# Optimization experiments

Hardware: AMD Instinct MI355X
Metric: run time of the kernel (lower is better)

The kernel has to match this reference:

```python
import jax, jax.numpy as jnp
import numpy as np

B, N, C, D = 2, 6, 64, 40
FH, FW = 12, 33
IMG_H, IMG_W = 384, 1056
NX, NY, NZ = 100, 100, 4
LOWER = np.array([-50.0, -50.0, -10.0], np.float32)   # xbound[0], ybound[0], zbound[0]
DXV = np.array([1.0, 1.0, 5.0], np.float32)           # voxel sizes


def _conv(x, w, pad):
    return jax.lax.conv_general_dilated(x, w, (1, 1), [(pad, pad), (pad, pad)],
                                        dimension_numbers=('NCHW', 'OIHW', 'NCHW'))


def _bn(x, s, b):
    return x * s[None, :, None, None] + b[None, :, None, None]


def _se(x, w1, b1, w2, b2):
    m = x.mean((2, 3))                                   # global avg pool -> (B, C)
    g = jax.nn.sigmoid(jax.nn.silu(m @ w1.T + b1) @ w2.T + b2)
    return x * g[:, :, None, None]


def _frustum():
    ds = jnp.arange(4.0, 44.0, 1.0)                      # (D,) depth bins
    xs = jnp.linspace(0.0, IMG_W - 1.0, FW)
    ys = jnp.linspace(0.0, IMG_H - 1.0, FH)
    f = jnp.stack(jnp.broadcast_arrays(xs[None, None, :], ys[None, :, None], ds[:, None, None]), -1)
    return f.reshape(-1, 3)                              # (D*FH*FW, 3) in (x_px, y_px, depth)


def reference(feats, rots, trans, intrinsics, nw1, bn1s, bn1b, se1w1, se1b1, se1w2, se1b2,
              nw2, bn2s, bn2b, dhw, dhb, chw, chb, bcw1, bcs1, bcb1, bcsw1, bcsb1, bcsw2,
              bcsb2, bcw2, bcs2, bcb2, dw1, ds1, db1, dw2, db2):
    BN = B * N
    # ---- CamEncoderV2 neck + heads (backbone 1280ch@1/32 features given directly) ----
    x = jax.nn.silu(_bn(_conv(feats, nw1, 0), bn1s, bn1b))
    x = _se(x, se1w1, se1b1, se1w2, se1b2)
    x = jax.nn.silu(_bn(_conv(x, nw2, 1), bn2s, bn2b))
    depth = jax.nn.softmax(_conv(x, dhw, 0) + dhb[None, :, None, None], axis=1)  # (BN, D, FH, FW)
    ctx = _conv(x, chw, 0) + chb[None, :, None, None]                            # (BN, C, FH, FW)
    # ---- geometry: pixel frustum -> ego-frame points ----
    rots_f = rots.reshape(BN, 3, 3)
    trans_f = trans.reshape(BN, 3)
    K = intrinsics.reshape(BN, 3, 3)
    pts = _frustum()                                     # (P0, 3), P0 = D*FH*FW
    d = pts[:, 2]
    fx, fy = K[:, 0, 0][:, None], K[:, 1, 1][:, None]
    cx, cy = K[:, 0, 2][:, None], K[:, 1, 2][:, None]
    cam = jnp.stack([(pts[None, :, 0] - cx) * d[None, :] / fx,
                     (pts[None, :, 1] - cy) * d[None, :] / fy,
                     jnp.broadcast_to(d[None, :], (BN, d.shape[0]))], -1)        # (BN, P0, 3)
    geom = jnp.einsum('bij,bpj->bpi', rots_f, cam) + trans_f[:, None, :]
    geom = geom.reshape(B, -1, 3)                        # (B, N*P0, 3)
    # ---- lift: outer product context x depth ----
    ff = (ctx[:, None, :, :, :] * depth[:, :, None, :, :])                       # (BN, D, C, FH, FW)
    ff = ff.transpose(0, 1, 3, 4, 2).reshape(B, -1, C)                           # (B, N*P0, C)
    # ---- splat: voxel pooling (scatter-add into BEV grid) ----
    idx = jnp.floor((geom - jnp.asarray(LOWER)) / jnp.asarray(DXV)).astype(jnp.int32)
    valid = jnp.all((idx >= 0) & (idx < jnp.array([NX, NY, NZ])), axis=-1)
    sid = idx[..., 2] * (NX * NY) + idx[..., 0] * NY + idx[..., 1]
    sid = jnp.where(valid, sid, 0)
    ffm = ff * valid[..., None]
    pooled = jax.vmap(lambda f, i: jax.ops.segment_sum(f, i, num_segments=NZ * NX * NY))(ffm, sid)
    bev = pooled.reshape(B, NZ, NX, NY, C).transpose(0, 1, 4, 2, 3).reshape(B, NZ * C, NX, NY)
    # ---- BEVCompressorV2 (residual conv-SE-conv) ----
    h = jax.nn.relu(_bn(_conv(bev, bcw1, 1), bcs1, bcb1))
    h = _se(h, bcsw1, bcsb1, bcsw2, bcsb2)
    h = jax.nn.relu(_bn(_conv(h, bcw2, 1), bcs2, bcb2))
    bev = bev + h
    # ---- decoder ----
    h = jax.nn.relu(_bn(_conv(bev, dw1, 1), ds1, db1))
    out = _conv(h, dw2, 0) + db2[None, :, None, None]    # (B, nz*num_classes, NX, NY)
    return out.reshape(B, 4, NZ, NX, NY)


def setup_inputs():
    f32 = jnp.float32
    ks = jax.random.split(jax.random.key(0), 16)
    feats = jax.random.normal(ks[0], (B * N, 1280, FH, FW), f32) * 0.5
    # cam->ego: z_cam -> x_ego, -x_cam -> y_ego, -y_cam -> z_ego, plus per-camera yaw
    Rbase = np.array([[0., 0., 1.], [-1., 0., 0.], [0., -1., 0.]], np.float32)
    yaw = np.deg2rad(np.arange(N) * 60.0).astype(np.float32)
    c, s = np.cos(yaw), np.sin(yaw)
    Rz = np.zeros((N, 3, 3), np.float32)
    Rz[:, 0, 0] = c; Rz[:, 0, 1] = -s; Rz[:, 1, 0] = s; Rz[:, 1, 1] = c; Rz[:, 2, 2] = 1.0
    rots = jnp.asarray(np.broadcast_to(np.einsum('nij,jk->nik', Rz, Rbase), (B, N, 3, 3)).copy())
    trans = jax.random.normal(ks[1], (B, N, 3), f32) * 1.0
    K = np.array([[800., 0., 528.], [0., 800., 192.], [0., 0., 1.]], np.float32)
    intrinsics = jnp.asarray(np.broadcast_to(K, (B, N, 3, 3)).copy())

    def w(k, shape, fan_in):
        return jax.random.normal(k, shape, f32) * np.float32(np.sqrt(2.0 / fan_in))

    kk = jax.random.split(ks[2], 16)
    return dict(
        feats=feats, rots=rots, trans=trans, intrinsics=intrinsics,
        nw1=w(kk[0], (256, 1280, 1, 1), 1280), bn1s=jnp.ones(256, f32), bn1b=jnp.zeros(256, f32),
        se1w1=w(kk[1], (32, 256), 256), se1b1=jnp.zeros(32, f32),
        se1w2=w(kk[2], (256, 32), 32), se1b2=jnp.zeros(256, f32),
        nw2=w(kk[3], (256, 256, 3, 3), 2304), bn2s=jnp.ones(256, f32), bn2b=jnp.zeros(256, f32),
        dhw=w(kk[4], (40, 256, 1, 1), 256), dhb=jnp.zeros(40, f32),
        chw=w(kk[5], (64, 256, 1, 1), 256), chb=jnp.zeros(64, f32),
        bcw1=w(kk[6], (256, 256, 3, 3), 2304), bcs1=jnp.ones(256, f32), bcb1=jnp.zeros(256, f32),
        bcsw1=w(kk[7], (16, 256), 256), bcsb1=jnp.zeros(16, f32),
        bcsw2=w(kk[8], (256, 16), 16), bcsb2=jnp.zeros(256, f32),
        bcw2=w(kk[9], (256, 256, 3, 3), 2304), bcs2=jnp.ones(256, f32), bcb2=jnp.zeros(256, f32),
        dw1=w(kk[10], (128, 256, 3, 3), 2304), ds1=jnp.ones(128, f32), db1=jnp.zeros(128, f32),
        dw2=w(kk[11], (16, 128, 1, 1), 128), db2=jnp.zeros(16, f32),
    )
```

## Files before the change

### kernel.cpp

```cpp
#include <hip/hip_runtime.h>
#include <hip/hip_bf16.h>
#include <cmath>


typedef __attribute__((ext_vector_type(8))) short short8;
typedef __attribute__((ext_vector_type(4))) float floatx4;
typedef __hip_bfloat16 hb;

__device__ __forceinline__ float sigf(float x){ return 1.0f/(1.0f+expf(-x)); }
__device__ __forceinline__ float siluf(float x){ return x*sigf(x); }
__device__ __forceinline__ void split2(float v, hb* h, hb* l){
  hb hv = __float2bfloat16(v);
  *h = hv; *l = __float2bfloat16(v - __bfloat162float(hv));
}

__global__ __launch_bounds__(256) void k_trans_featsP(
    const float* __restrict__ feats, hb* __restrict__ Fph, hb* __restrict__ Fpl)
{
  __shared__ float tile[64][65];
  int n = blockIdx.z;
  int p0 = blockIdx.x*64;
  int c0 = blockIdx.y*64;
  int tid = threadIdx.x;
  int tr = tid >> 6;
  int tc = tid & 63;
  #pragma unroll
  for (int it=0; it<16; ++it){
    int ci = c0 + it*4 + tr;
    int p = p0 + tc;
    float v = 0.f;
    if (p < 396) v = feats[((size_t)n*1280 + ci)*396 + p];
    tile[it*4+tr][tc] = v;
  }
  __syncthreads();
  #pragma unroll
  for (int iter=0; iter<2; ++iter){
    int idx = iter*256 + tid;
    int oc = idx >> 6;
    int pl = idx & 63;
    int p = p0 + pl;
    if (p < 396){
      int P = n*396 + p;
      int T = P >> 4, mm = P & 15;
      int kb = (c0 >> 5) + (oc >> 2);
      int q = oc & 3;
      int lane = q*16 + mm;
      size_t o = (((size_t)T*40 + kb)*64 + lane)*8;
      #pragma unroll
      for (int j=0; j<8; ++j){
        hb hv, lv; split2(tile[oc*8+j][pl], &hv, &lv);
        Fph[o+j] = hv; Fpl[o+j] = lv;
      }
    }
  }
}

__global__ __launch_bounds__(256) void k_wpackE(
    const float* __restrict__ nw1, const float* __restrict__ nw2,
    hb* __restrict__ Wc1h, hb* __restrict__ Wc1l,
    hb* __restrict__ Wc2h, hb* __restrict__ Wc2l)
{
  int i = blockIdx.x*256 + threadIdx.x;
  if (i < 327680){
    int j = i & 7;
    int lane = (i>>3) & 63;
    int t2 = i >> 9;
    int nb = t2 & 15;
    int kb = t2 >> 4;
    int ci = kb*32 + (lane>>4)*8 + j;
    int co = nb*16 + (lane&15);
    hb hv, lv; split2(nw1[(size_t)co*1280 + ci], &hv, &lv);
    Wc1h[i] = hv; Wc1l[i] = lv;
  } else {
    int i2 = i - 327680;
    if (i2 >= 589824) return;
    int j = i2 & 7;
    int t1 = i2 >> 3;
    int lane = t1 & 63;
    int t2 = t1 >> 6;
    int nb = t2 % 16;
    int t3 = t2 / 16;
    int tap = t3 % 9;
    int kb = t3 / 9;
    int ci = kb*32 + (lane>>4)*8 + j;
    int co = nb*16 + (lane&15);
    hb hv, lv; split2(nw2[(size_t)co*2304 + ci*9 + tap], &hv, &lv);
    Wc2h[i2] = hv; Wc2l[i2] = lv;
  }
}

__global__ __launch_bounds__(256) void k_wpackT3(
    const float* __restrict__ bcw1, const float* __restrict__ bcw2,
    const float* __restrict__ dw1,
    hb* __restrict__ W1h, hb* __restrict__ W1l,
    hb* __restrict__ W2h, hb* __restrict__ W2l,
    hb* __restrict__ W3h, hb* __restrict__ W3l)
{
  int gi = blockIdx.x*256 + threadIdx.x;
  const float* W; hb* Wh; hb* Wl; int NB; int i;
  if (gi < 589824){ W = bcw1; Wh = W1h; Wl = W1l; NB = 16; i = gi; }
  else if (gi < 1179648){ W = bcw2; Wh = W2h; Wl = W2l; NB = 16; i = gi - 589824; }
  else if (gi < 1474560){ W = dw1; Wh = W3h; Wl = W3l; NB = 8; i = gi - 1179648; }
  else return;
  int j = i & 7;
  int t1 = i >> 3;
  int lane = t1 & 63;
  int t2 = t1 >> 6;
  int nb = t2 % NB;
  int t3 = t2 / NB;
  int tap = t3 % 9;
  int kb = t3 / 9;
  int ci = kb*32 + (lane>>4)*8 + j;
  int co = nb*16 + (lane&15);
  hb hv, lv; split2(W[(size_t)co*2304 + ci*9 + tap], &hv, &lv);
  Wh[i] = hv; Wl[i] = lv;
}

__global__ __launch_bounds__(256) void k_wpackH(
    const float* __restrict__ dhw, const float* __restrict__ chw,
    hb* __restrict__ Wph, hb* __restrict__ Wpl)
{
  int i = blockIdx.x*256 + threadIdx.x;
  if (i >= 8*7*512) return;
  int j = i & 7;
  int t1 = i >> 3;
  int lane = t1 & 63;
  int t2 = t1 >> 6;
  int nb = t2 % 7;
  int kb = t2 / 7;
  int ci = kb*32 + (lane>>4)*8 + j;
  int co = nb*16 + (lane&15);
  float w = 0.f;
  if (co < 40) w = dhw[(size_t)co*256 + ci];
  else if (co < 104) w = chw[(size_t)(co-40)*256 + ci];
  hb hv, lv; split2(w, &hv, &lv);
  Wph[i] = hv; Wpl[i] = lv;
}

__global__ __launch_bounds__(256) void k_mfma_gemm1(
    const hb* __restrict__ Fph, const hb* __restrict__ Fpl,
    const hb* __restrict__ Wph, const hb* __restrict__ Wpl,
    const float* __restrict__ bns, const float* __restrict__ bnb,
    float* __restrict__ out)
{
  __shared__ short8 lbh[256], lbl[256];
  int tid = threadIdx.x;
  int wv = tid >> 6, lane = tid & 63;
  int cog = blockIdx.y;
  int Pbase = blockIdx.x*128 + wv*32;
  int q = lane >> 4;
  int T0 = blockIdx.x*8 + wv*2; if (T0 > 296) T0 = 296;
  int T1 = T0 + 1;              if (T1 > 296) T1 = 296;
  size_t a0 = (size_t)T0*2560 + lane;
  size_t a1 = (size_t)T1*2560 + lane;
  const short8* gAh = (const short8*)(const void*)Fph;
  const short8* gAl = (const short8*)(const void*)Fpl;
  const short8* gWh = (const short8*)(const void*)Wph;
  const short8* gWl = (const short8*)(const void*)Wpl;
  size_t sb = (size_t)(cog*4 + wv)*64 + lane;
  floatx4 acc[2][4];
  #pragma unroll
  for (int i=0;i<2;++i)
    #pragma unroll
    for (int j=0;j<4;++j) acc[i][j] = (floatx4)(0.f);
  short8 ph = gWh[sb], pw = gWl[sb];
  short8 cah0 = gAh[a0], cal0 = gAl[a0], cah1 = gAh[a1], cal1 = gAl[a1];
  for (int kb=0; kb<40; ++kb){
    __syncthreads();
    lbh[tid] = ph; lbl[tid] = pw;
    int nx = (kb+1 < 40) ? kb+1 : 39;
    ph = gWh[(size_t)nx*1024 + sb]; pw = gWl[(size_t)nx*1024 + sb];
    __syncthreads();
    short8 nah0 = gAh[a0 + (size_t)nx*64];
    short8 nal0 = gAl[a0 + (size_t)nx*64];
    short8 nah1 = gAh[a1 + (size_t)nx*64];
    short8 nal1 = gAl[a1 + (size_t)nx*64];
    #pragma unroll
    for (int nb=0; nb<4; ++nb){
      short8 bh = lbh[nb*64 + lane];
      short8 bl = lbl[nb*64 + lane];
      acc[0][nb] = __builtin_amdgcn_mfma_f32_16x16x32_bf16(cah0, bh, acc[0][nb], 0,0,0);
      acc[0][nb] = __builtin_amdgcn_mfma_f32_16x16x32_bf16(cah0, bl, acc[0][nb], 0,0,0);
      acc[0][nb] = __builtin_amdgcn_mfma_f32_16x16x32_bf16(cal0, bh, acc[0][nb], 0,0,0);
      acc[1][nb] = __builtin_amdgcn_mfma_f32_16x16x32_bf16(cah1, bh, acc[1][nb], 0,0,0);
      acc[1][nb] = __builtin_amdgcn_mfma_f32_16x16x32_bf16(cah1, bl, acc[1][nb], 0,0,0);
      acc[1][nb] = __builtin_amdgcn_mfma_f32_16x16x32_bf16(cal1, bh, acc[1][nb], 0,0,0);
    }
    cah0 = nah0; cal0 = nal0; cah1 = nah1; cal1 = nal1;
  }
  int n16 = lane & 15;
  #pragma unroll
  for (int mg=0; mg<2; ++mg){
    #pragma unroll
    for (int nb=0; nb<4; ++nb){
      int co = cog*64 + nb*16 + n16;
      float s = bns[co], bv = bnb[co];
      #pragma unroll
      for (int r=0; r<4; ++r){
        int P = Pbase + mg*16 + q*4 + r;
        if (P < 4752) out[(size_t)P*256 + co] = siluf(acc[mg][nb][r]*s + bv);
      }
    }
  }
}

__global__ __launch_bounds__(256) void k_meanse(
    const float* __restrict__ x1, const float* __restrict__ w1, const float* __restrict__ b1,
    const float* __restrict__ w2, const float* __restrict__ b2, float* __restrict__ g)
{
  __shared__ float m[256];
  __shared__ float h[32];
  int n = blockIdx.x; int t = threadIdx.x;
  float s = 0.f;
  for (int p=0; p<396; ++p) s += x1[((size_t)n*396+p)*256 + t];
  m[t] = s*(1.f/396.f);
  __syncthreads();
  if (t < 32){
    float s2 = b1[t];
    for (int c=0; c<256; ++c) s2 += m[c]*w1[t*256+c];
    h[t] = siluf(s2);
  }
  __syncthreads();
  float s3 = b2[t];
  for (int j=0; j<32; ++j) s3 += h[j]*w2[t*32+j];
  g[n*256+t] = sigf(s3);
}

__global__ __launch_bounds__(256) void k_se_fc(
    const float* __restrict__ mean, const float* __restrict__ w1, const float* __restrict__ b1,
    const float* __restrict__ w2, const float* __restrict__ b2, float* __restrict__ g, int H)
{
  __shared__ float m[256];
  __shared__ float h[32];
  int n = blockIdx.x; int t = threadIdx.x;
  m[t] = mean[n*256 + t];
  __syncthreads();
  if (t < H){
    float s = b1[t];
    for (int c=0; c<256; ++c) s += m[c]*w1[t*256+c];
    h[t] = siluf(s);
  }
  __syncthreads();
  float s = b2[t];
  for (int j=0; j<H; ++j) s += h[j]*w2[t*H+j];
  g[n*256+t] = sigf(s);
}

__global__ __launch_bounds__(256) void k_topad(
    const float* __restrict__ x1, const float* __restrict__ g,
    hb* __restrict__ Xh, hb* __restrict__ Xl)
{
  int y = blockIdx.x;
  int n = blockIdx.y;
  int c = threadIdx.x;
  float gc = g[n*256+c];
  for (int xx=0; xx<35; ++xx){
    float v = 0.f;
    if (y>=1 && y<=12 && xx>=1 && xx<=33)
      v = x1[((size_t)n*396 + (y-1)*33 + (xx-1))*256 + c]*gc;
    hb hv, lv; split2(v, &hv, &lv);
    size_t o = (((size_t)n*14+y)*35+xx)*256 + c;
    Xh[o] = hv; Xl[o] = lv;
  }
}

__global__ __launch_bounds__(256) void k_conv3_img(
    const hb* __restrict__ Xh, const hb* __restrict__ Xl,
    const hb* __restrict__ Wph, const hb* __restrict__ Wpl,
    const float* __restrict__ bns, const float* __restrict__ bnb,
    hb* __restrict__ outh, hb* __restrict__ outl)
{
  __shared__ __align__(16) short sAh[10*18*44];
  __shared__ __align__(16) short sAl[10*18*44];
  __shared__ short8 lbh[2][256], lbl[2][256];
  int tid = threadIdx.x;
  int wv = tid >> 6, lane = tid & 63;
  int xg = blockIdx.x;
  int n = blockIdx.y >> 1, yg = blockIdx.y & 1;
  int cog = blockIdx.z;
  int x0 = xg*16;
  int y0 = yg*8 + wv;
  int m = lane & 15, q = lane >> 4;
  floatx4 acc[2][4];
  #pragma unroll
  for (int i=0;i<2;++i)
    #pragma unroll
    for (int j=0;j<4;++j) acc[i][j] = (floatx4)(0.f);

  const short8* gAh = (const short8*)(const void*)Xh;
  const short8* gAl = (const short8*)(const void*)Xl;
  const short8* gWh = (const short8*)(const void*)Wph;
  const short8* gWl = (const short8*)(const void*)Wpl;
  const size_t sb = (size_t)(cog*4 + wv)*64 + lane;
  const size_t nbase = (size_t)n*14*35*32;

  short8 ph = gWh[sb], pl = gWl[sb];
  int cur = 0;

  for (int kb=0; kb<8; ++kb){
    #pragma unroll 3
    for (int tap=0; tap<9; ++tap){
      int idx2 = kb*9 + tap;
      if (tap == 0){
        __syncthreads();
        for (int i = tid; i < 720; i += 256){
          int rc = i >> 2, part = i & 3;
          int r = rc / 18, c2 = rc % 18;
          int yr = yg*8 + r; if (yr > 13) yr = 13;
          int xc = x0 + c2;  if (xc > 34) xc = 34;
          size_t so = nbase + (size_t)(yr*35 + xc)*32 + kb*4 + part;
          short8 vh = gAh[so], vl = gAl[so];
          int dst = (r*18 + c2)*44 + part*8;
          *(short8*)(sAh + dst) = vh;
          *(short8*)(sAl + dst) = vl;
        }
      }
      lbh[cur][tid] = ph; lbl[cur][tid] = pl;
      int nx = (idx2+1 < 72) ? idx2+1 : 71;
      ph = gWh[(size_t)nx*1024 + sb];
      pl = gWl[(size_t)nx*1024 + sb];
      __syncthreads();
      int dy = (tap*11) >> 5;
      int dx = tap - dy*3;
      int cc = dx + m;
      int a0 = ((wv + dy)*18 + cc)*44 + q*8;
      int a1 = ((wv + 4 + dy)*18 + cc)*44 + q*8;
      short8 cah0 = *(const short8*)(sAh + a0);
      short8 cal0 = *(const short8*)(sAl + a0);
      short8 cah1 = *(const short8*)(sAh + a1);
      short8 cal1 = *(const short8*)(sAl + a1);
      #pragma unroll
      for (int nb=0; nb<4; ++nb){
        short8 bh = lbh[cur][nb*64 + lane];
        short8 bl = lbl[cur][nb*64 + lane];
        acc[0][nb] = __builtin_amdgcn_mfma_f32_16x16x32_bf16(cah0, bh, acc[0][nb], 0,0,0);
        acc[0][nb] = __builtin_amdgcn_mfma_f32_16x16x32_bf16(cah0, bl, acc[0][nb], 0,0,0);
        acc[0][nb] = __builtin_amdgcn_mfma_f32_16x16x32_bf16(cal0, bh, acc[0][nb], 0,0,0);
        acc[1][nb] = __builtin_amdgcn_mfma_f32_16x16x32_bf16(cah1, bh, acc[1][nb], 0,0,0);
        acc[1][nb] = __builtin_amdgcn_mfma_f32_16x16x32_bf16(cah1, bl, acc[1][nb], 0,0,0);
        acc[1][nb] = __builtin_amdgcn_mfma_f32_16x16x32_bf16(cal1, bh, acc[1][nb], 0,0,0);
      }
      cur ^= 1;
    }
  }

  int n16 = lane & 15;
  #pragma unroll
  for (int mg=0; mg<2; ++mg){
    int oy = y0 + mg*4;
    if (oy < 12){
      #pragma unroll
      for (int r=0; r<4; ++r){
        int ox = x0 + q*4 + r;
        if (ox < 33){
          int P = n*396 + oy*33 + ox;
          #pragma unroll
          for (int nb=0; nb<4; ++nb){
            int co = cog*64 + nb*16 + n16;
            float v = siluf(acc[mg][nb][r]*bns[co] + bnb[co]);
            hb hv, lv; split2(v, &hv, &lv);
            outh[(size_t)P*256 + co] = hv;
            outl[(size_t)P*256 + co] = lv;
          }
        }
      }
    }
  }
}

__global__ __launch_bounds__(256) void k_headsM(
    const hb* __restrict__ x2h, const hb* __restrict__ x2l,
    const hb* __restrict__ Whh, const hb* __restrict__ Whl,
    const float* __restrict__ dhb, const float* __restrict__ chb,
    float* __restrict__ dep, float* __restrict__ ctx2)
{
  __shared__ short8 lbh[256], lbl[256];
  int tid = threadIdx.x;
  int wv = tid >> 6, lane = tid & 63;
  int cog = blockIdx.y;
  int nb0 = cog*4;
  int nbN = cog ? 3 : 4;
  int Pbase = blockIdx.x*128 + wv*32;
  int m = lane & 15, q = lane >> 4;
  int P0 = Pbase + m;      if (P0 > 4751) P0 = 4751;
  int P1 = Pbase + 16 + m; if (P1 > 4751) P1 = 4751;
  size_t rA0 = (size_t)P0*32 + q;
  size_t rA1 = (size_t)P1*32 + q;
  const short8* gAh = (const short8*)(const void*)x2h;
  const short8* gAl = (const short8*)(const void*)x2l;
  const short8* gWh = (const short8*)(const void*)Whh;
  const short8* gWl = (const short8*)(const void*)Whl;
  floatx4 acc[2][4];
  #pragma unroll
  for (int i=0;i<2;++i)
    #pragma unroll
    for (int j=0;j<4;++j) acc[i][j] = (floatx4)(0.f);
  for (int kb=0; kb<8; ++kb){
    __syncthreads();
    for (int i=tid; i<nbN*64; i+=256){
      lbh[i] = gWh[(size_t)(kb*7 + nb0)*64 + i];
      lbl[i] = gWl[(size_t)(kb*7 + nb0)*64 + i];
    }
    __syncthreads();
    short8 ah0 = gAh[rA0 + kb*4], al0 = gAl[rA0 + kb*4];
    short8 ah1 = gAh[rA1 + kb*4], al1 = gAl[rA1 + kb*4];
    for (int nb=0; nb<nbN; ++nb){
      short8 bh = lbh[nb*64 + lane];
      short8 bl = lbl[nb*64 + lane];
      acc[0][nb] = __builtin_amdgcn_mfma_f32_16x16x32_bf16(ah0, bh, acc[0][nb], 0,0,0);
      acc[0][nb] = __builtin_amdgcn_mfma_f32_16x16x32_bf16(ah0, bl, acc[0][nb], 0,0,0);
      acc[0][nb] = __builtin_amdgcn_mfma_f32_16x16x32_bf16(al0, bh, acc[0][nb], 0,0,0);
      acc[1][nb] = __builtin_amdgcn_mfma_f32_16x16x32_bf16(ah1, bh, acc[1][nb], 0,0,0);
      acc[1][nb] = __builtin_amdgcn_mfma_f32_16x16x32_bf16(ah1, bl, acc[1][nb], 0,0,0);
      acc[1][nb] = __builtin_amdgcn_mfma_f32_16x16x32_bf16(al1, bh, acc[1][nb], 0,0,0);
    }
  }
  int n16 = lane & 15;
  #pragma unroll
  for (int mg=0; mg<2; ++mg){
    #pragma unroll
    for (int r=0; r<4; ++r){
      int P = Pbase + mg*16 + q*4 + r;
      if (P < 4752){
        int nn = P/396, pim = P%396;
        for (int nb=0; nb<nbN; ++nb){
          int co = cog*64 + nb*16 + n16;
          float v = acc[mg][nb][r];
          if (co < 40)
            dep[((size_t)nn*40 + co)*396 + pim] = v + dhb[co];
          else if (co < 104)
            ctx2[((size_t)nn*396 + pim)*64 + (co-40)] = v + chb[co-40];
        }
      }
    }
  }
}

__global__ __launch_bounds__(256) void k_softmax40(float* __restrict__ dep)
{
  int i = blockIdx.x*256 + threadIdx.x;
  if (i >= 12*396) return;
  int n = i/396, p = i%396;
  float* base = dep + (size_t)n*40*396 + p;
  float mx = -1e30f;
  for (int d=0; d<40; ++d) mx = fmaxf(mx, base[(size_t)d*396]);
  float s = 0.f;
  for (int d=0; d<40; ++d){ float e = expf(base[(size_t)d*396]-mx); base[(size_t)d*396]=e; s+=e; }
  float inv = 1.f/s;
  for (int d=0; d<40; ++d) base[(size_t)d*396] *= inv;
}

__global__ __launch_bounds__(256) void k_geom(
    const float* __restrict__ rots, const float* __restrict__ trans,
    const float* __restrict__ intr, int* __restrict__ vox, int* __restrict__ cnt)
{
  int pt = blockIdx.x*256 + threadIdx.x;
  if (pt >= 190080) return;
  int b = pt/95040; int r = pt%95040;
  int n = r/15840;  int r2 = r%15840;
  int d = r2/396;   int pim = r2%396;
  int y = pim/33, x = pim%33;
  int bn = b*6+n;
  const float* R = rots + (size_t)bn*9;
  const float* T = trans + (size_t)bn*3;
  const float* K = intr + (size_t)bn*9;
  float fx=K[0], cx=K[2], fy=K[4], cy=K[5];
  float xs = (float)x * 32.96875f;
  float ys = (float)((double)y * (383.0/11.0));
  float dv = 4.0f + (float)d;
  float camx = (xs-cx)*dv/fx;
  float camy = (ys-cy)*dv/fy;
  float gx = R[0]*camx + R[1]*camy + R[2]*dv + T[0];
  float gy = R[3]*camx + R[4]*camy + R[5]*dv + T[1];
  float gz = R[6]*camx + R[7]*camy + R[8]*dv + T[2];
  int ix = (int)floorf(gx + 50.f);
  int iy = (int)floorf(gy + 50.f);
  int iz = (int)floorf((gz + 10.f)/5.f);
  bool valid = (ix>=0 && ix<100 && iy>=0 && iy<100 && iz>=0 && iz<4);
  int sid = iz*10000 + ix*100 + iy;
  vox[pt] = valid ? sid : -1;
  if (valid) atomicAdd(&cnt[b*40000 + sid], 1);
}

__global__ __launch_bounds__(256) void k_scan1(
    const int* __restrict__ cnt, int* __restrict__ off, int* __restrict__ bsum)
{
  __shared__ int s[256];
  int t = threadIdx.x;
  int i = blockIdx.x*256 + t;
  int v = (i < 80000) ? cnt[i] : 0;
  s[t] = v; __syncthreads();
  for (int o=1;o<256;o<<=1){
    int x = (t>=o) ? s[t-o] : 0;
    __syncthreads();
    s[t] += x;
    __syncthreads();
  }
  if (i < 80000) off[i] = s[t] - v;
  if (t == 255) bsum[blockIdx.x] = s[255];
}

__global__ void k_scan2(int* __restrict__ bsum, int nblk)
{
  int lane = threadIdx.x & 63;
  int run = 0;
  for (int base=0; base<nblk; base+=64){
    int i = base + lane;
    int v = (i < nblk) ? bsum[i] : 0;
    int s = v;
    #pragma unroll
    for (int o=1;o<64;o<<=1){
      int t = __shfl_up(s, o);
      if (lane >= o) s += t;
    }
    int total = __shfl(s, 63);
    if (i < nblk) bsum[i] = run + s - v;
    run += total;
  }
}

__global__ __launch_bounds__(256) void k_scan3(
    int* __restrict__ off, const int* __restrict__ bsum, int* __restrict__ cur)
{
  int i = blockIdx.x*256 + threadIdx.x;
  if (i >= 80000) return;
  int o = off[i] + bsum[i>>8];
  off[i] = o;
  cur[i] = o;
}

__global__ __launch_bounds__(256) void k_fill(
    const int* __restrict__ vox, int* __restrict__ cur, int* __restrict__ list)
{
  int pt = blockIdx.x*256 + threadIdx.x;
  if (pt >= 190080) return;
  int s = vox[pt];
  if (s < 0) return;
  int b = pt/95040;
  int slot = atomicAdd(&cur[b*40000 + s], 1);
  list[slot] = pt;
}

__global__ __launch_bounds__(256) void k_zero_ring(hb* __restrict__ Ah, hb* __restrict__ Al)
{
  int i = blockIdx.x*256 + threadIdx.x;
  if (i >= 2*404*256) return;
  int c = i & 255;
  int t = i >> 8;
  int b = t / 404;
  int ridx = t % 404;
  int py, px;
  if (ridx < 102){ py = 0; px = ridx; }
  else if (ridx < 204){ py = 101; px = ridx-102; }
  else if (ridx < 304){ py = ridx-204+1; px = 0; }
  else { py = ridx-304+1; px = 101; }
  size_t o = (((size_t)b*102 + py)*102 + px)*256 + c;
  hb z = __float2bfloat16(0.f);
  Ah[o] = z; Al[o] = z;
}

__global__ __launch_bounds__(256) void k_gather(
    const int* __restrict__ off, const int* __restrict__ cnt, const int* __restrict__ list,
    const float* __restrict__ ctx2, const float* __restrict__ dep, float* __restrict__ bev,
    hb* __restrict__ Ah, hb* __restrict__ Al)
{
  int tid = threadIdx.x;
  int bv = blockIdx.x*4 + (tid>>6);
  int c = tid & 63;
  int b = bv/40000, sid = bv%40000;
  int st = off[bv], nn = cnt[bv];
  float s = 0.f;
  for (int k=0;k<nn;++k){
    int pt = list[st+k];
    int r = pt%95040;
    int bn = b*6 + r/15840;
    int r2 = r%15840;
    int dd = r2/396, pim = r2%396;
    s += ctx2[((size_t)bn*396+pim)*64 + c] * dep[((size_t)bn*40+dd)*396 + pim];
  }
  int iz = sid/10000, rem = sid%10000;
  bev[(size_t)b*2560000 + (size_t)iz*640000 + (size_t)c*10000 + rem] = s;
  int ix = rem/100, iy = rem%100;
  size_t oh = (((size_t)b*102 + (ix+1))*102 + (iy+1))*256 + iz*64 + c;
  hb hv, lv; split2(s, &hv, &lv);
  Ah[oh] = hv; Al[oh] = lv;
}

__global__ __launch_bounds__(256) void k_tohwc2(
    const float* __restrict__ in, hb* __restrict__ Ah, hb* __restrict__ Al,
    const float* __restrict__ g)
{
  __shared__ float tile[32*105];
  int py = blockIdx.x;
  int b  = blockIdx.y;
  int cg = blockIdx.z;
  int tid = threadIdx.x;
  bool inner = (py >= 1 && py <= 100);
  if (inner){
    if (tid < 64){ int cil = tid & 31; int col = (tid>>5) ? 101 : 0; tile[cil*105 + col] = 0.f; }
    for (int i = tid; i < 3200; i += 256){
      int cil = i / 100, x = i % 100;
      int ci = cg*32 + cil;
      tile[cil*105 + (x+1)] = in[(((size_t)b*256 + ci)*100 + (py-1))*100 + x];
    }
  }
  __syncthreads();
  for (int i = tid; i < 32*102; i += 256){
    int px = i >> 5, cil = i & 31;
    int ci = cg*32 + cil;
    float v = 0.f;
    if (inner){
      v = tile[cil*105 + px];
      if (g) v *= g[b*256 + ci];
    }
    hb hv, lv; split2(v, &hv, &lv);
    size_t o = (((size_t)b*102 + py)*102 + px)*256 + ci;
    Ah[o] = hv; Al[o] = lv;
  }
}

__global__ __launch_bounds__(256) void k_rowmean(
    const float* __restrict__ in, float* __restrict__ out, int rowlen, float inv)
{
  __shared__ float ws[4];
  int row = blockIdx.x; int t = threadIdx.x;
  const float* p = in + (size_t)row*rowlen;
  float s = 0.f;
  for (int i=t; i<rowlen; i+=256) s += p[i];
  #pragma unroll
  for (int off=32; off; off>>=1) s += __shfl_down(s, off);
  if ((t&63)==0) ws[t>>6] = s;
  __syncthreads();
  if (t==0) out[row] = (ws[0]+ws[1]+ws[2]+ws[3]) * inv;
}

__global__ __launch_bounds__(256) void k_conv3_bevm(
    const hb* __restrict__ Ah, const hb* __restrict__ Al,
    const hb* __restrict__ Wph, const hb* __restrict__ Wpl,
    const float* __restrict__ bns, const float* __restrict__ bnb,
    const float* __restrict__ res, float* __restrict__ out, int Cout, int NBG)
{
  __shared__ __align__(16) short sAh[10*18*44];
  __shared__ __align__(16) short sAl[10*18*44];
  const int NB = Cout >> 4;
  int tid = threadIdx.x;
  int wv = tid >> 6, lane = tid & 63;
  int wc = wv & 1;
  int wy = wv >> 1;
  int L = blockIdx.x;
  int spatial = L / (NBG*2);
  int rem = L % (NBG*2);
  int cog = rem % NBG;
  int bb  = rem / NBG;
  int xg = spatial % 7, yg = spatial / 7;
  int x0 = xg*16;
  int m = lane & 15, q = lane >> 4;
  int nb0 = cog*4 + wc*2;
  floatx4 acc[4][2];
  #pragma unroll
  for (int r=0;r<4;++r)
    #pragma unroll
    for (int u=0;u<2;++u) acc[r][u] = (floatx4)(0.f);

  const short8* gAh = (const short8*)(const void*)Ah;
  const short8* gAl = (const short8*)(const void*)Al;
  const short8* gWh = (const short8*)(const void*)Wph;
  const short8* gWl = (const short8*)(const void*)Wpl;
  const size_t nbstride = (size_t)NB*64;

  short8 pbh[2], pbl[2];
  #pragma unroll
  for (int u=0;u<2;++u){
    pbh[u] = gWh[(size_t)(nb0+u)*64 + lane];
    pbl[u] = gWl[(size_t)(nb0+u)*64 + lane];
  }

  for (int kb=0; kb<8; ++kb){
    __syncthreads();
    for (int i = tid; i < 720; i += 256){
      int rc = i >> 2, part = i & 3;
      int r = rc / 18, c = rc % 18;
      int yr = yg*8 + r; if (yr > 101) yr = 101;
      int xc = x0 + c;   if (xc > 101) xc = 101;
      size_t so = ((size_t)((bb*102 + yr)*102 + xc))*32 + kb*4 + part;
      short8 vh = gAh[so], vl = gAl[so];
      int dst = (r*18 + c)*44 + part*8;
      *(short8*)(sAh + dst) = vh;
      *(short8*)(sAl + dst) = vl;
    }
    __syncthreads();
    #pragma unroll 3
    for (int tap=0; tap<9; ++tap){
      int idx2 = kb*9 + tap;
      short8 cbh0 = pbh[0], cbh1 = pbh[1];
      short8 cbl0 = pbl[0], cbl1 = pbl[1];
      int nx = (idx2+1 < 72) ? idx2+1 : 71;
      #pragma unroll
      for (int u=0;u<2;++u){
        pbh[u] = gWh[(size_t)nx*nbstride + (size_t)(nb0+u)*64 + lane];
        pbl[u] = gWl[(size_t)nx*nbstride + (size_t)(nb0+u)*64 + lane];
      }
      int dy = (tap*11) >> 5;
      int dx = tap - dy*3;
      int cc = dx + m;
      #pragma unroll
      for (int r=0; r<4; ++r){
        int a0 = ((wy*4 + r + dy)*18 + cc)*44 + q*8;
        short8 cah = *(const short8*)(sAh + a0);
        short8 cal = *(const short8*)(sAl + a0);
        acc[r][0] = __builtin_amdgcn_mfma_f32_16x16x32_bf16(cah, cbh0, acc[r][0], 0,0,0);
        acc[r][0] = __builtin_amdgcn_mfma_f32_16x16x32_bf16(cah, cbl0, acc[r][0], 0,0,0);
        acc[r][0] = __builtin_amdgcn_mfma_f32_16x16x32_bf16(cal, cbh0, acc[r][0], 0,0,0);
        acc[r][1] = __builtin_amdgcn_mfma_f32_16x16x32_bf16(cah, cbh1, acc[r][1], 0,0,0);
        acc[r][1] = __builtin_amdgcn_mfma_f32_16x16x32_bf16(cah, cbl1, acc[r][1], 0,0,0);
        acc[r][1] = __builtin_amdgcn_mfma_f32_16x16x32_bf16(cal, cbh1, acc[r][1], 0,0,0);
      }
    }
  }

  int n = lane & 15;
  int xq = x0 + q*4;
  #pragma unroll
  for (int r=0; r<4; ++r){
    int yo = yg*8 + wy*4 + r;
    if (yo < 100 && xq < 100){
      #pragma unroll
      for (int u=0; u<2; ++u){
        int co = (nb0+u)*16 + n;
        float s = bns[co], bv = bnb[co];
        floatx4 a = acc[r][u];
        float4 v;
        v.x = fmaxf(a[0]*s+bv, 0.f);
        v.y = fmaxf(a[1]*s+bv, 0.f);
        v.z = fmaxf(a[2]*s+bv, 0.f);
        v.w = fmaxf(a[3]*s+bv, 0.f);
        size_t o = ((size_t)(bb*Cout+co)*100 + yo)*100 + xq;
        if (res){
          float4 rv = *(const float4*)(res + o);
          v.x += rv.x; v.y += rv.y; v.z += rv.z; v.w += rv.w;
        }
        *(float4*)(out + o) = v;
      }
    }
  }
}

__global__ __launch_bounds__(256) void k_final2(
    const float* __restrict__ h, const float* __restrict__ W, const float* __restrict__ bias,
    float* __restrict__ out)
{
  __shared__ float wsl[2048];
  __shared__ float bs[16];
  int tid = threadIdx.x;
  int b = blockIdx.y;
  for (int i=tid; i<2048; i+=256) wsl[i] = W[i];
  if (tid < 16) bs[tid] = bias[tid];
  __syncthreads();
  int pix = blockIdx.x*256 + tid;
  if (pix >= 10000) return;
  float acc[16];
  #pragma unroll
  for (int oc=0; oc<16; ++oc) acc[oc] = bs[oc];
  const float* hb_ = h + (size_t)b*128*10000 + pix;
  for (int ci=0; ci<128; ++ci){
    float hv = hb_[(size_t)ci*10000];
    #pragma unroll
    for (int oc=0; oc<16; ++oc) acc[oc] += hv * wsl[oc*128 + ci];
  }
  #pragma unroll
  for (int oc=0; oc<16; ++oc)
    out[((size_t)(b*16+oc))*10000 + pix] = acc[oc];
}

extern "C" void kernel_launch(void* const* d_in, const int* in_sizes, int n_in,
                              void* d_out, int out_size, void* d_ws, size_t ws_size,
                              hipStream_t stream)
{
  (void)in_sizes; (void)n_in; (void)out_size; (void)ws_size;
  const float* feats = (const float*)d_in[0];
  const float* rots  = (const float*)d_in[1];
  const float* trans = (const float*)d_in[2];
  const float* intr  = (const float*)d_in[3];
  const float* nw1   = (const float*)d_in[4];
  const float* bn1s  = (const float*)d_in[5];
  const float* bn1b  = (const float*)d_in[6];
  const float* se1w1 = (const float*)d_in[7];
  const float* se1b1 = (const float*)d_in[8];
  const float* se1w2 = (const float*)d_in[9];
  const float* se1b2 = (const float*)d_in[10];
  const float* nw2   = (const float*)d_in[11];
  const float* bn2s  = (const float*)d_in[12];
  const float* bn2b  = (const float*)d_in[13];
  const float* dhw   = (const float*)d_in[14];
  const float* dhb   = (const float*)d_in[15];
  const float* chw   = (const float*)d_in[16];
  const float* chb   = (const float*)d_in[17];
  const float* bcw1  = (const float*)d_in[18];
  const float* bcs1  = (const float*)d_in[19];
  const float* bcb1  = (const float*)d_in[20];
  const float* bcsw1 = (const float*)d_in[21];
  const float* bcsb1 = (const float*)d_in[22];
  const float* bcsw2 = (const float*)d_in[23];
  const float* bcsb2 = (const float*)d_in[24];
  const float* bcw2  = (const float*)d_in[25];
  const float* bcs2  = (const float*)d_in[26];
  const float* bcb2  = (const float*)d_in[27];
  const float* dw1   = (const float*)d_in[28];
  const float* ds1   = (const float*)d_in[29];
  const float* db1   = (const float*)d_in[30];
  const float* dw2   = (const float*)d_in[31];
  const float* db2   = (const float*)d_in[32];
  float* out = (float*)d_out;

  float* ws = (float*)d_ws;
  float* bev   = ws;
  float* h1    = ws + 5120000;
  hb*    Ah    = (hb*)(ws + 10240000);
  hb*    Al    = (hb*)(ws + 12903424);
  float* x2    = ws + 15566848;
  float* S5    = ws + 16783360;
  float* dep   = ws + 17373184;
  float* ctx2  = ws + 17563264;
  float* mean1 = ws + 17867392;
  float* g1    = mean1 + 3072;
  float* mean2 = g1 + 3072;
  float* g2    = mean2 + 512;
  int*   vox   = (int*)(ws + 17875584);
  hb* Fph  = (hb*)bev;
  hb* Wc1h = (hb*)(bev + 3041280);
  hb* Wc1l = (hb*)(bev + 3205120);
  float* x1 = h1;
  hb* Fpl  = (hb*)(h1 + 1216512);
  hb* Xh   = (hb*)Ah;
  hb* Xl   = (hb*)Al;
  hb* Wc2h = (hb*)S5;
  hb* Wc2l = (hb*)(S5 + 294912);
  hb* x2h  = (hb*)x2;
  hb* x2l  = (hb*)(x2 + 608256);
  hb* Whh  = (hb*)S5;
  hb* Whl  = (hb*)(S5 + 14336);
  int* cnt  = (int*)h1;
  int* off  = cnt + 80000;
  int* cur  = off + 80000;
  int* bsum = cur + 80000;
  int* list = bsum + 1024;
  float* h3 = h1;
  hb* Wp1h = (hb*)x2;
  hb* Wp1l = (hb*)(x2 + 294912);
  hb* Wp3h = (hb*)(x2 + 589824);
  hb* Wp3l = (hb*)(x2 + 589824 + 147456);
  hb* Wp2h = (hb*)S5;
  hb* Wp2l = (hb*)(S5 + 294912);

  k_trans_featsP<<<dim3(7,20,12),256,0,stream>>>(feats,Fph,Fpl);
  k_wpackE<<<3584,256,0,stream>>>(nw1,nw2,Wc1h,Wc1l,Wc2h,Wc2l);
  k_mfma_gemm1<<<dim3(38,4),256,0,stream>>>(Fph,Fpl,Wc1h,Wc1l,bn1s,bn1b,x1);
  k_meanse<<<12,256,0,stream>>>(x1,se1w1,se1b1,se1w2,se1b2,g1);
  k_topad<<<dim3(14,12),256,0,stream>>>(x1,g1,Xh,Xl);
  k_conv3_img<<<dim3(3,24,4),256,0,stream>>>(Xh,Xl,Wc2h,Wc2l,bn2s,bn2b,x2h,x2l);
  k_wpackH<<<112,256,0,stream>>>(dhw,chw,Whh,Whl);
  k_headsM<<<dim3(38,2),256,0,stream>>>(x2h,x2l,Whh,Whl,dhb,chb,dep,ctx2);
  k_softmax40<<<19,256,0,stream>>>(dep);

  k_wpackT3<<<5760,256,0,stream>>>(bcw1,bcw2,dw1,Wp1h,Wp1l,Wp2h,Wp2l,Wp3h,Wp3l);

  hipMemsetAsync(cnt, 0, 80000*sizeof(int), stream);
  k_geom<<<(190080+255)/256,256,0,stream>>>(rots,trans,intr,vox,cnt);
  k_scan1<<<313,256,0,stream>>>(cnt,off,bsum);
  k_scan2<<<1,64,0,stream>>>(bsum,313);
  k_scan3<<<(80000+255)/256,256,0,stream>>>(off,bsum,cur);
  k_fill<<<(190080+255)/256,256,0,stream>>>(vox,cur,list);
  k_zero_ring<<<808,256,0,stream>>>(Ah,Al);
  k_gather<<<20000,256,0,stream>>>(off,cnt,list,ctx2,dep,bev,Ah,Al);

  k_conv3_bevm<<<728,256,0,stream>>>(Ah,Al,Wp1h,Wp1l,bcs1,bcb1,nullptr,h1,256,4);
  k_rowmean<<<512,256,0,stream>>>(h1,mean2,10000,1e-4f);
  k_se_fc<<<2,256,0,stream>>>(mean2,bcsw1,bcsb1,bcsw2,bcsb2,g2,16);
  k_tohwc2<<<dim3(102,2,8),256,0,stream>>>(h1,Ah,Al,g2);
  k_conv3_bevm<<<728,256,0,stream>>>(Ah,Al,Wp2h,Wp2l,bcs2,bcb2,bev,bev,256,4);
  k_tohwc2<<<dim3(102,2,8),256,0,stream>>>(bev,Ah,Al,nullptr);
  k_conv3_bevm<<<364,256,0,stream>>>(Ah,Al,Wp3h,Wp3l,ds1,db1,nullptr,h3,128,2);
  k_final2<<<dim3(40,2),256,0,stream>>>(h3,dw2,db2,out);
}
```

Measured before the change: 631.4 us.

## Switch BEV intermediates to NHWC and precompute per-slot depth in fill

The BEV-stage float intermediates (bev, h1) now use a channel-last layout instead of NCHW. Channel-wise repacking into the padded bf16 hi/lo buffers becomes a simple coalesced copy with no shared-memory transpose, and the SE mean becomes a column reduction using atomics. The fill kernel now stores a flattened pixel index plus the gathered depth probability per slot, so the gather loop drops its div/mod work and does one fewer indirect load; that loop is also unrolled by two. Tradeoffs: the conv epilogue now writes strided scalar stores instead of float4, the mean adds a memset and atomics, and depv needs extra scratch space placed after the list.

```diff
diff --git a/kernel.cpp b/kernel.cpp
--- a/kernel.cpp
+++ b/kernel.cpp
@@ -530,15 +530,20 @@
 }
 
 __global__ __launch_bounds__(256) void k_fill(
-    const int* __restrict__ vox, int* __restrict__ cur, int* __restrict__ list)
+    const int* __restrict__ vox, int* __restrict__ cur, int* __restrict__ list,
+    const float* __restrict__ dep, float* __restrict__ depv)
 {
   int pt = blockIdx.x*256 + threadIdx.x;
   if (pt >= 190080) return;
   int s = vox[pt];
   if (s < 0) return;
-  int b = pt/95040;
+  int b = pt/95040; int r = pt%95040;
+  int bn = b*6 + r/15840;
+  int r2 = r%15840;
+  int dd = r2/396, pim = r2%396;
   int slot = atomicAdd(&cur[b*40000 + s], 1);
-  list[slot] = pt;
+  list[slot] = bn*396 + pim;
+  depv[slot] = dep[((size_t)bn*40 + dd)*396 + pim];
 }
 
 __global__ __launch_bounds__(256) void k_zero_ring(hb* __restrict__ Ah, hb* __restrict__ Al)
@@ -561,8 +566,8 @@
 
 __global__ __launch_bounds__(256) void k_gather(
     const int* __restrict__ off, const int* __restrict__ cnt, const int* __restrict__ list,
-    const float* __restrict__ ctx2, const float* __restrict__ dep, float* __restrict__ bev,
-    hb* __restrict__ Ah, hb* __restrict__ Al)
+    const float* __restrict__ depv, const float* __restrict__ ctx2,
+    float* __restrict__ bev, hb* __restrict__ Ah, hb* __restrict__ Al)
 {
   int tid = threadIdx.x;
   int bv = blockIdx.x*4 + (tid>>6);
@@ -570,75 +575,60 @@
   int b = bv/40000, sid = bv%40000;
   int st = off[bv], nn = cnt[bv];
   float s = 0.f;
-  for (int k=0;k<nn;++k){
-    int pt = list[st+k];
-    int r = pt%95040;
-    int bn = b*6 + r/15840;
-    int r2 = r%15840;
-    int dd = r2/396, pim = r2%396;
-    s += ctx2[((size_t)bn*396+pim)*64 + c] * dep[((size_t)bn*40+dd)*396 + pim];
-  }
+  int k = 0;
+  for (; k+2 <= nn; k += 2){
+    int p0 = list[st+k], p1 = list[st+k+1];
+    float d0 = depv[st+k], d1 = depv[st+k+1];
+    float c0 = ctx2[(size_t)p0*64 + c];
+    float c1 = ctx2[(size_t)p1*64 + c];
+    s += c0*d0 + c1*d1;
+  }
+  if (k < nn)
+    s += ctx2[(size_t)list[st+k]*64 + c] * depv[st+k];
   int iz = sid/10000, rem = sid%10000;
-  bev[(size_t)b*2560000 + (size_t)iz*640000 + (size_t)c*10000 + rem] = s;
+  bev[((size_t)b*10000 + rem)*256 + iz*64 + c] = s;
   int ix = rem/100, iy = rem%100;
   size_t oh = (((size_t)b*102 + (ix+1))*102 + (iy+1))*256 + iz*64 + c;
   hb hv, lv; split2(s, &hv, &lv);
   Ah[oh] = hv; Al[oh] = lv;
 }
 
-__global__ __launch_bounds__(256) void k_tohwc2(
-    const float* __restrict__ in, hb* __restrict__ Ah, hb* __restrict__ Al,
-    const float* __restrict__ g)
-{
-  __shared__ float tile[32*105];
-  int py = blockIdx.x;
-  int b  = blockIdx.y;
-  int cg = blockIdx.z;
-  int tid = threadIdx.x;
-  bool inner = (py >= 1 && py <= 100);
-  if (inner){
-    if (tid < 64){ int cil = tid & 31; int col = (tid>>5) ? 101 : 0; tile[cil*105 + col] = 0.f; }
-    for (int i = tid; i < 3200; i += 256){
-      int cil = i / 100, x = i % 100;
-      int ci = cg*32 + cil;
-      tile[cil*105 + (x+1)] = in[(((size_t)b*256 + ci)*100 + (py-1))*100 + x];
-    }
-  }
-  __syncthreads();
-  for (int i = tid; i < 32*102; i += 256){
-    int px = i >> 5, cil = i & 31;
-    int ci = cg*32 + cil;
-    float v = 0.f;
-    if (inner){
-      v = tile[cil*105 + px];
-      if (g) v *= g[b*256 + ci];
-    }
+__global__ __launch_bounds__(256) void k_packA(
+    const float* __restrict__ src, const float* __restrict__ g,
+    hb* __restrict__ Ah, hb* __restrict__ Al)
+{
+  int ix = blockIdx.x;
+  int b = blockIdx.z;
+  int c = threadIdx.x;
+  float gc = g ? g[b*256 + c] : 1.f;
+  #pragma unroll
+  for (int i=0; i<4; ++i){
+    int iy = blockIdx.y*4 + i;
+    float v = src[((size_t)b*10000 + ix*100 + iy)*256 + c] * gc;
     hb hv, lv; split2(v, &hv, &lv);
-    size_t o = (((size_t)b*102 + py)*102 + px)*256 + ci;
+    size_t o = (((size_t)b*102 + ix+1)*102 + iy+1)*256 + c;
     Ah[o] = hv; Al[o] = lv;
   }
 }
 
-__global__ __launch_bounds__(256) void k_rowmean(
-    const float* __restrict__ in, float* __restrict__ out, int rowlen, float inv)
-{
-  __shared__ float ws[4];
-  int row = blockIdx.x; int t = threadIdx.x;
-  const float* p = in + (size_t)row*rowlen;
+__global__ __launch_bounds__(256) void k_mean_nhwc(
+    const float* __restrict__ h1, float* __restrict__ mean2)
+{
+  int chunk = blockIdx.x;
+  int b = blockIdx.y;
+  int c = threadIdx.x;
   float s = 0.f;
-  for (int i=t; i<rowlen; i+=256) s += p[i];
-  #pragma unroll
-  for (int off=32; off; off>>=1) s += __shfl_down(s, off);
-  if ((t&63)==0) ws[t>>6] = s;
-  __syncthreads();
-  if (t==0) out[row] = (ws[0]+ws[1]+ws[2]+ws[3]) * inv;
+  for (int p=0; p<250; ++p)
+    s += h1[((size_t)b*10000 + chunk*250 + p)*256 + c];
+  atomicAdd(&mean2[b*256 + c], s*1e-4f);
 }
 
 __global__ __launch_bounds__(256) void k_conv3_bevm(
     const hb* __restrict__ Ah, const hb* __restrict__ Al,
     const hb* __restrict__ Wph, const hb* __restrict__ Wpl,
     const float* __restrict__ bns, const float* __restrict__ bnb,
-    const float* __restrict__ res, float* __restrict__ out, int Cout, int NBG)
+    const float* __restrict__ resN, float* __restrict__ outF, int outNCHW,
+    int Cout, int NBG)
 {
   __shared__ __align__(16) short sAh[10*18*44];
   __shared__ __align__(16) short sAl[10*18*44];
@@ -729,17 +719,27 @@
         int co = (nb0+u)*16 + n;
         float s = bns[co], bv = bnb[co];
         floatx4 a = acc[r][u];
-        float4 v;
-        v.x = fmaxf(a[0]*s+bv, 0.f);
-        v.y = fmaxf(a[1]*s+bv, 0.f);
-        v.z = fmaxf(a[2]*s+bv, 0.f);
-        v.w = fmaxf(a[3]*s+bv, 0.f);
-        size_t o = ((size_t)(bb*Cout+co)*100 + yo)*100 + xq;
-        if (res){
-          float4 rv = *(const float4*)(res + o);
-          v.x += rv.x; v.y += rv.y; v.z += rv.z; v.w += rv.w;
+        float v0 = fmaxf(a[0]*s+bv, 0.f);
+        float v1 = fmaxf(a[1]*s+bv, 0.f);
+        float v2 = fmaxf(a[2]*s+bv, 0.f);
+        float v3 = fmaxf(a[3]*s+bv, 0.f);
+        if (outNCHW){
+          float4 v; v.x=v0; v.y=v1; v.z=v2; v.w=v3;
+          size_t o = ((size_t)(bb*Cout+co)*100 + yo)*100 + xq;
+          *(float4*)(outF + o) = v;
+        } else {
+          size_t base = ((size_t)bb*10000 + yo*100 + xq)*256 + co;
+          if (resN){
+            v0 += resN[base];
+            v1 += resN[base+256];
+            v2 += resN[base+512];
+            v3 += resN[base+768];
+          }
+          outF[base]     = v0;
+          outF[base+256] = v1;
+          outF[base+512] = v2;
+          outF[base+768] = v3;
         }
-        *(float4*)(out + o) = v;
       }
     }
   }
@@ -844,6 +844,7 @@
   int* cur  = off + 80000;
   int* bsum = cur + 80000;
   int* list = bsum + 1024;
+  float* depv = (float*)(list + 190080);
   float* h3 = h1;
   hb* Wp1h = (hb*)x2;
   hb* Wp1l = (hb*)(x2 + 294912);
@@ -869,16 +870,17 @@
   k_scan1<<<313,256,0,stream>>>(cnt,off,bsum);
   k_scan2<<<1,64,0,stream>>>(bsum,313);
   k_scan3<<<(80000+255)/256,256,0,stream>>>(off,bsum,cur);
-  k_fill<<<(190080+255)/256,256,0,stream>>>(vox,cur,list);
+  k_fill<<<(190080+255)/256,256,0,stream>>>(vox,cur,list,dep,depv);
   k_zero_ring<<<808,256,0,stream>>>(Ah,Al);
-  k_gather<<<20000,256,0,stream>>>(off,cnt,list,ctx2,dep,bev,Ah,Al);
-
-  k_conv3_bevm<<<728,256,0,stream>>>(Ah,Al,Wp1h,Wp1l,bcs1,bcb1,nullptr,h1,256,4);
-  k_rowmean<<<512,256,0,stream>>>(h1,mean2,10000,1e-4f);
+  k_gather<<<20000,256,0,stream>>>(off,cnt,list,depv,ctx2,bev,Ah,Al);
+
+  k_conv3_bevm<<<728,256,0,stream>>>(Ah,Al,Wp1h,Wp1l,bcs1,bcb1,nullptr,h1,0,256,4);
+  hipMemsetAsync(mean2, 0, 512*sizeof(float), stream);
+  k_mean_nhwc<<<dim3(40,2),256,0,stream>>>(h1,mean2);
   k_se_fc<<<2,256,0,stream>>>(mean2,bcsw1,bcsb1,bcsw2,bcsb2,g2,16);
-  k_tohwc2<<<dim3(102,2,8),256,0,stream>>>(h1,Ah,Al,g2);
-  k_conv3_bevm<<<728,256,0,stream>>>(Ah,Al,Wp2h,Wp2l,bcs2,bcb2,bev,bev,256,4);
-  k_tohwc2<<<dim3(102,2,8),256,0,stream>>>(bev,Ah,Al,nullptr);
-  k_conv3_bevm<<<364,256,0,stream>>>(Ah,Al,Wp3h,Wp3l,ds1,db1,nullptr,h3,128,2);
+  k_packA<<<dim3(100,25,2),256,0,stream>>>(h1,g2,Ah,Al);
+  k_conv3_bevm<<<728,256,0,stream>>>(Ah,Al,Wp2h,Wp2l,bcs2,bcb2,bev,bev,0,256,4);
+  k_packA<<<dim3(100,25,2),256,0,stream>>>(bev,nullptr,Ah,Al);
+  k_conv3_bevm<<<364,256,0,stream>>>(Ah,Al,Wp3h,Wp3l,ds1,db1,nullptr,h3,1,128,2);
   k_final2<<<dim3(40,2),256,0,stream>>>(h3,dw2,db2,out);
 }
```

New measurement: 581.5 us. -7.9%, faster.
